# Performance work log

Hardware: AMD Instinct MI355X
Metric: run time of the kernel (lower is better)

The kernel has to match this reference:

```python
import jax, jax.numpy as jnp
import numpy as np

D_MODEL = 768
D_STATE = 128
EXPAND = 2
HEADDIM = 64
D_INNER = D_MODEL * EXPAND          # 1536
NHEADS = D_INNER // HEADDIM         # 24
CONV_K = 4
D_IN_PROJ = 2 * D_INNER + 2 * D_STATE + NHEADS  # z, xBC, dt
EPS = 1e-5


def setup_inputs() -> dict:
    key = jax.random.key(0)
    ks = jax.random.split(key, 12)
    B, L = 4, 4096
    conv_ch = D_INNER + 2 * D_STATE
    inp = {
        "x": jax.random.normal(ks[0], (B, L, D_MODEL), dtype=jnp.float32),
        "ln_w": jnp.ones((D_MODEL,), jnp.float32),
        "ln_b": jnp.zeros((D_MODEL,), jnp.float32),
        "W_in": jax.random.normal(ks[1], (D_MODEL, D_IN_PROJ), jnp.float32) * (D_MODEL ** -0.5),
        "conv_w": jax.random.normal(ks[2], (conv_ch, 1, CONV_K), jnp.float32) * (CONV_K ** -0.5),
        "conv_b": jnp.zeros((conv_ch,), jnp.float32),
        "A_log": jnp.log(jnp.arange(1, NHEADS + 1, dtype=jnp.float32)),
        "D": jnp.ones((NHEADS,), jnp.float32),
        "dt_bias": jnp.log(jnp.expm1(jax.random.uniform(ks[3], (NHEADS,), jnp.float32, 1e-3, 0.1))),
        "norm_w": jnp.ones((D_INNER,), jnp.float32),
        "W_out": jax.random.normal(ks[4], (D_INNER, D_MODEL), jnp.float32) * (D_INNER ** -0.5),
    }
    return inp


def _layernorm(x, w, b):
    mu = jnp.mean(x, -1, keepdims=True)
    var = jnp.mean(jnp.square(x - mu), -1, keepdims=True)
    return (x - mu) * jax.lax.rsqrt(var + EPS) * w + b


def _causal_dw_conv(x, w, b):
    # x: (B, L, C), w: (C, 1, K) depthwise causal conv
    xt = jnp.transpose(x, (0, 2, 1))                      # (B, C, L)
    xt = jnp.pad(xt, ((0, 0), (0, 0), (CONV_K - 1, 0)))
    y = jax.lax.conv_general_dilated(
        xt, w, window_strides=(1,), padding="VALID",
        dimension_numbers=("NCH", "OIH", "NCH"),
        feature_group_count=x.shape[-1])
    return jnp.transpose(y, (0, 2, 1)) + b                # (B, L, C)


def _mamba_core(u, W_in, conv_w, conv_b, A_log, D, dt_bias, norm_w, W_out):
    Bsz, L, _ = u.shape
    zxbcdt = u @ W_in                                      # (B, L, D_IN_PROJ)
    z = zxbcdt[..., :D_INNER]
    xBC = zxbcdt[..., D_INNER:D_INNER + D_INNER + 2 * D_STATE]
    dt = zxbcdt[..., -NHEADS:]                             # (B, L, H)

    xBC = jax.nn.silu(_causal_dw_conv(xBC, conv_w, conv_b))
    xs = xBC[..., :D_INNER].reshape(Bsz, L, NHEADS, HEADDIM)   # (B,L,H,P)
    Bmat = xBC[..., D_INNER:D_INNER + D_STATE]                 # (B,L,N)
    Cmat = xBC[..., D_INNER + D_STATE:]                        # (B,L,N)

    dt = jax.nn.softplus(dt + dt_bias)                     # (B,L,H)
    A = -jnp.exp(A_log)                                    # (H,)
    dA = jnp.exp(dt * A)                                   # (B,L,H)

    def step(h, inputs):
        dA_t, dt_t, B_t, C_t, x_t = inputs                 # (B,H),(B,H),(B,N),(B,N),(B,H,P)
        h = dA_t[:, :, None, None] * h + \
            (dt_t[:, :, None] * x_t)[..., None] * B_t[:, None, None, :]
        y = jnp.einsum("bhpn,bn->bhp", h, C_t)
        return h, y

    h0 = jnp.zeros((Bsz, NHEADS, HEADDIM, D_STATE), u.dtype)
    seq = (jnp.moveaxis(dA, 1, 0), jnp.moveaxis(dt, 1, 0),
           jnp.moveaxis(Bmat, 1, 0), jnp.moveaxis(Cmat, 1, 0),
           jnp.moveaxis(xs, 1, 0))
    _, ys = jax.lax.scan(step, h0, seq)                    # (L,B,H,P)
    y = jnp.moveaxis(ys, 0, 1) + D[None, None, :, None] * xs
    y = y.reshape(Bsz, L, D_INNER)

    # gated RMSNorm then out projection
    yg = y * jax.nn.silu(z)
    yn = yg * jax.lax.rsqrt(jnp.mean(jnp.square(yg), -1, keepdims=True) + EPS) * norm_w
    return yn @ W_out


def reference(x, ln_w, ln_b, W_in, conv_w, conv_b, A_log, D, dt_bias, norm_w, W_out):
    u = _layernorm(x, ln_w, ln_b)
    out = _mamba_core(u, W_in, conv_w, conv_b, A_log, D, dt_bias, norm_w, W_out)
    return out + x  # dropout p=0.0 is identity
```

## Files before the change

kernel.cpp:

```cpp
#include <hip/hip_runtime.h>
#include <stdint.h>

#define B_SZ 4
#define LSEQ 4096
#define DMODEL 768
#define DSTATE 128
#define HEADD 64
#define DINNER 1536
#define NH 24
#define NPROJ 3352
#define NPROJ_PAD 3456
#define NXBC 1920
#define ROWS (B_SZ*LSEQ)
#define QC 64
#define NGRP 8
#define GQ 8
#define GLEN (GQ*QC)

typedef __attribute__((ext_vector_type(8))) short short8;
typedef __attribute__((ext_vector_type(4))) float floatx4;

__device__ __forceinline__ unsigned short f2bf(float f){
  union { float f; unsigned u; } v; v.f = f;
  unsigned r = v.u + 0x7FFFu + ((v.u >> 16) & 1u);
  return (unsigned short)(r >> 16);
}
__device__ __forceinline__ float bf2f(unsigned short u){
  union { unsigned u; float f; } v; v.u = ((unsigned)u) << 16; return v.f;
}
__device__ __forceinline__ float silu(float v){ return v / (1.f + __expf(-v)); }

__global__ __launch_bounds__(256) void transpose_bf16(const float* __restrict__ src, int R, int C,
                                                      unsigned short* __restrict__ dst){
  __shared__ __align__(16) float tile[32][33];
  int tx = threadIdx.x & 31, ty = threadIdx.x >> 5;
  int n0 = blockIdx.x * 32, k0 = blockIdx.y * 32;
  #pragma unroll
  for (int i = 0; i < 4; i++){
    int k = k0 + ty + i*8, n = n0 + tx;
    tile[ty + i*8][tx] = (n < C) ? src[(size_t)k * C + n] : 0.f;
  }
  __syncthreads();
  #pragma unroll
  for (int i = 0; i < 4; i++){
    int n = n0 + ty + i*8, k = k0 + tx;
    dst[(size_t)n * R + k] = f2bf(tile[tx][ty + i*8]);
  }
}

__global__ __launch_bounds__(256) void ln_kernel(const float* __restrict__ x, const float* __restrict__ w,
                                                 const float* __restrict__ b, unsigned short* __restrict__ u){
  int row = blockIdx.x, t = threadIdx.x;
  const float* xr = x + (size_t)row * DMODEL;
  float v0 = xr[t], v1 = xr[t+256], v2 = xr[t+512];
  float s = v0+v1+v2, ss = v0*v0+v1*v1+v2*v2;
  __shared__ float sa[4], sb[4];
  #pragma unroll
  for (int o = 32; o > 0; o >>= 1){ s += __shfl_down(s,o,64); ss += __shfl_down(ss,o,64); }
  if ((t & 63) == 0){ sa[t>>6] = s; sb[t>>6] = ss; }
  __syncthreads();
  s = sa[0]+sa[1]+sa[2]+sa[3]; ss = sb[0]+sb[1]+sb[2]+sb[3];
  float mu = s * (1.f/DMODEL);
  float var = ss * (1.f/DMODEL) - mu*mu;
  float rs = rsqrtf(var + 1e-5f);
  unsigned short* ur = u + (size_t)row * DMODEL;
  ur[t]     = f2bf((v0-mu)*rs*w[t]     + b[t]);
  ur[t+256] = f2bf((v1-mu)*rs*w[t+256] + b[t+256]);
  ur[t+512] = f2bf((v2-mu)*rs*w[t+512] + b[t+512]);
}

#define SSTR 1040
#define GEMM_CORE(A_, Bt_, K_)                                                          \
  __shared__ __align__(16) short As[4*SSTR];                                            \
  __shared__ __align__(16) short Bs[4*SSTR];                                            \
  int t = threadIdx.x;                                                                  \
  int bm = blockIdx.y, bn = blockIdx.x;                                                 \
  int wave = t >> 6, lane = t & 63;                                                     \
  int wr = wave >> 1, wc = wave & 1;                                                    \
  int q = lane >> 4, m16 = lane & 15;                                                   \
  floatx4 acc[4][4];                                                                    \
  _Pragma("unroll") for (int i=0;i<4;i++)                                               \
    _Pragma("unroll") for (int j=0;j<4;j++) acc[i][j] = (floatx4){0.f,0.f,0.f,0.f};     \
  const int r0 = t >> 2, s0 = t & 3;                                                    \
  for (int kt = 0; kt < (K_); kt += 32){                                                \
    uint4 av0 = *(const uint4*)((A_)  + (size_t)(bm*128 + r0     )*(K_) + kt + s0*8);   \
    uint4 av1 = *(const uint4*)((A_)  + (size_t)(bm*128 + r0 + 64)*(K_) + kt + s0*8);   \
    uint4 bv0 = *(const uint4*)((Bt_) + (size_t)(bn*128 + r0     )*(K_) + kt + s0*8);   \
    uint4 bv1 = *(const uint4*)((Bt_) + (size_t)(bn*128 + r0 + 64)*(K_) + kt + s0*8);   \
    *(uint4*)(As + s0*SSTR + r0*8)      = av0;                                          \
    *(uint4*)(As + s0*SSTR + (r0+64)*8) = av1;                                          \
    *(uint4*)(Bs + s0*SSTR + r0*8)      = bv0;                                          \
    *(uint4*)(Bs + s0*SSTR + (r0+64)*8) = bv1;                                          \
    __syncthreads();                                                                    \
    short8 af[4], bf_[4];                                                               \
    _Pragma("unroll") for (int i=0;i<4;i++){                                            \
      af[i]  = *(const short8*)(As + q*SSTR + (wr*64 + i*16 + m16)*8);                  \
      bf_[i] = *(const short8*)(Bs + q*SSTR + (wc*64 + i*16 + m16)*8);                  \
    }                                                                                   \
    _Pragma("unroll") for (int i=0;i<4;i++)                                             \
      _Pragma("unroll") for (int j=0;j<4;j++)                                           \
        acc[i][j] = __builtin_amdgcn_mfma_f32_16x16x32_bf16(af[i], bf_[j], acc[i][j], 0, 0, 0); \
    __syncthreads();                                                                    \
  }

__global__ __launch_bounds__(256) void gemm_in(const short* __restrict__ A, const short* __restrict__ Bt,
                                               unsigned short* __restrict__ zb, unsigned short* __restrict__ xb,
                                               float* __restrict__ dtb, const float* __restrict__ dt_bias){
  GEMM_CORE(A, Bt, DMODEL)
  #pragma unroll
  for (int i=0;i<4;i++){
    int grow_base = bm*128 + wr*64 + i*16 + q*4;
    #pragma unroll
    for (int j=0;j<4;j++){
      int gcol = bn*128 + wc*64 + j*16 + m16;
      #pragma unroll
      for (int r=0;r<4;r++){
        int row = grow_base + r;
        float v = acc[i][j][r];
        if (gcol < DINNER){
          zb[(size_t)row*DINNER + gcol] = f2bf(v);
        } else {
          xb[(size_t)row*NXBC + (gcol - DINNER)] = f2bf(v);
          if (gcol >= (NPROJ-NH) && gcol < NPROJ){
            int hh = gcol - (NPROJ-NH);
            float xr = v + dt_bias[hh];
            dtb[(size_t)row*NH + hh] = (xr > 20.f) ? xr : log1pf(expf(xr));
          }
        }
      }
    }
  }
}

__global__ __launch_bounds__(256) void gemm_out(const short* __restrict__ A, const short* __restrict__ Bt,
                                                float* __restrict__ C, const float* __restrict__ resid){
  GEMM_CORE(A, Bt, DINNER)
  #pragma unroll
  for (int i=0;i<4;i++){
    int grow_base = bm*128 + wr*64 + i*16 + q*4;
    #pragma unroll
    for (int j=0;j<4;j++){
      int gcol = bn*128 + wc*64 + j*16 + m16;
      #pragma unroll
      for (int r=0;r<4;r++){
        size_t idx = (size_t)(grow_base + r) * DMODEL + gcol;
        C[idx] = acc[i][j][r] + resid[idx];
      }
    }
  }
}

__global__ __launch_bounds__(256) void conv_bc(const unsigned short* __restrict__ xbc,
                                               const float* __restrict__ cw, const float* __restrict__ cb,
                                               unsigned short* __restrict__ bcv){
  int row = blockIdx.x, c = threadIdx.x;
  int l = row & (LSEQ-1);
  int chg = DINNER + c;
  float acc = cb[chg];
  #pragma unroll
  for (int k = 0; k < 4; k++){
    int ls = l + k - 3;
    if (ls >= 0) acc = fmaf(cw[chg*4+k], bf2f(xbc[(size_t)(row + k - 3)*NXBC + 1536 + c]), acc);
  }
  bcv[(size_t)row*256 + c] = f2bf(silu(acc));
}

__global__ __launch_bounds__(256, 2) void ssd_partial(const unsigned short* __restrict__ xbc,
                                                      const unsigned short* __restrict__ bcv,
                                                      const float* __restrict__ dtb,
                                                      const float* __restrict__ cw, const float* __restrict__ cb,
                                                      const float* __restrict__ A_log, const float* __restrict__ Dp,
                                                      unsigned short* __restrict__ yb,
                                                      unsigned short* __restrict__ gstate,
                                                      float* __restrict__ gamma){
  __shared__ __align__(16) unsigned short sBl[QC][136];
  __shared__ __align__(16) unsigned short sCl[QC][136];
  __shared__ __align__(16) unsigned short sXT[HEADD][72];
  __shared__ __align__(16) unsigned short sMR[67*72];
  __shared__ __align__(16) unsigned short sH[HEADD][136];
  __shared__ float sSeg[QC], sDt[QC], sW[QC], sCum[QC];

  int bid = blockIdx.x;
  int g = bid % NGRP, bh = bid / NGRP;
  int h = bh % NH, b = bh / NH;
  int bseq = b * LSEQ;
  int tid = threadIdx.x;
  int wv = tid >> 6, ln = tid & 63, q = ln >> 4, l16 = ln & 15;
  float A_h = -__expf(A_log[h]);
  float Dh = Dp[h];

  float cwr[4][4], cbr[4];
  #pragma unroll
  for (int sl = 0; sl < 4; sl++){
    int chg = h*HEADD + (tid>>4) + 16*sl;
    #pragma unroll
    for (int k = 0; k < 4; k++) cwr[sl][k] = cw[chg*4+k];
    cbr[sl] = cb[chg];
  }

  for (int i = tid; i < HEADD*136/2; i += 256) ((unsigned*)sH)[i] = 0u;
  floatx4 hacc[8];
  #pragma unroll
  for (int i = 0; i < 8; i++) hacc[i] = (floatx4){0.f,0.f,0.f,0.f};
  float segRun = 0.f;

  for (int cc = 0; cc < GQ; cc++){
    int l0 = g*GLEN + cc*QC;
    {
      int r = tid >> 2, gb = tid & 3;
      const unsigned short* bcrow = bcv + (size_t)(bseq + l0 + r)*256;
      uint4 bcl[8];
      #pragma unroll
      for (int j = 0; j < 8; j++) bcl[j] = *(const uint4*)(bcrow + (gb + 4*j)*8);
      uint4 rxl[3]; int rrow[3], rg[3]; bool rv[3];
      #pragma unroll
      for (int j = 0; j < 3; j++){
        int idx = tid + 256*j;
        rv[j] = idx < 536;
        int rr = idx >> 3, gg = idx & 7;
        rrow[j] = rr; rg[j] = gg;
        rxl[j] = (uint4){0,0,0,0};
        if (rv[j]){
          int gl = l0 + rr - 3;
          if (gl >= 0) rxl[j] = *(const uint4*)(xbc + (size_t)(bseq + gl)*NXBC + h*HEADD + gg*8);
        }
      }
      if (wv == 0){
        float dtv = dtb[(size_t)(bseq + l0 + ln)*NH + h];
        float sg = dtv * A_h;
        #pragma unroll
        for (int off = 1; off < 64; off <<= 1){
          float o = __shfl_up(sg, off, 64);
          sg += (ln >= off) ? o : 0.f;
        }
        float segLast = __shfl(sg, 63, 64);
        sSeg[ln] = sg; sDt[ln] = dtv;
        sW[ln] = dtv * __expf(segLast - sg);
        sCum[ln] = __expf(sg);
        gamma[(size_t)bh*LSEQ + l0 + ln] = __expf(segRun + sg);
        segRun += segLast;
      }
      #pragma unroll
      for (int j = 0; j < 8; j++){
        int ch0 = (gb + 4*j) * 8;
        if (ch0 < 128) *(uint4*)&sBl[r][ch0] = bcl[j];
        else           *(uint4*)&sCl[r][ch0-128] = bcl[j];
      }
      #pragma unroll
      for (int j = 0; j < 3; j++)
        if (rv[j]) *(uint4*)&sMR[rrow[j]*72 + rg[j]*8] = rxl[j];
    }
    __syncthreads();
    short8 cf[4];
    #pragma unroll
    for (int kt = 0; kt < 4; kt++) cf[kt] = *(const short8*)&sCl[16*wv + l16][kt*32 + q*8];
    floatx4 gacc[4];
    #pragma unroll
    for (int st = 0; st < 4; st++) gacc[st] = (floatx4){0.f,0.f,0.f,0.f};
    #pragma unroll
    for (int kt = 0; kt < 4; kt++){
      #pragma unroll
      for (int st = 0; st < 4; st++){
        short8 bfr = *(const short8*)&sBl[16*st + l16][kt*32 + q*8];
        gacc[st] = __builtin_amdgcn_mfma_f32_16x16x32_bf16(cf[kt], bfr, gacc[st], 0, 0, 0);
      }
    }
    {
      int s4 = (tid & 15) * 4;
      #pragma unroll
      for (int sl = 0; sl < 4; sl++){
        int ch = (tid >> 4) + 16*sl;
        float rr[7];
        #pragma unroll
        for (int k = 0; k < 7; k++) rr[k] = bf2f(sMR[(s4 + k)*72 + ch]);
        #pragma unroll
        for (int i = 0; i < 4; i++){
          float v = cbr[sl] + cwr[sl][0]*rr[i] + cwr[sl][1]*rr[i+1] + cwr[sl][2]*rr[i+2] + cwr[sl][3]*rr[i+3];
          sXT[ch][s4+i] = f2bf(silu(v));
        }
      }
    }
    __syncthreads();
    #pragma unroll
    for (int st = 0; st < 4; st++){
      #pragma unroll
      for (int r = 0; r < 4; r++){
        int tt = 16*wv + q*4 + r;
        int ss = 16*st + l16;
        float mv = 0.f;
        if (ss <= tt) mv = __expf(sSeg[tt] - sSeg[ss]) * sDt[ss] * gacc[st][r];
        sMR[tt*72 + ss] = f2bf(mv);
      }
    }
    __syncthreads();
    short8 xf[2][4];
    #pragma unroll
    for (int kt = 0; kt < 2; kt++)
      #pragma unroll
      for (int pt = 0; pt < 4; pt++)
        xf[kt][pt] = *(const short8*)&sXT[16*pt + l16][kt*32 + q*8];
    floatx4 yac[4], y2[4];
    #pragma unroll
    for (int pt = 0; pt < 4; pt++){ yac[pt] = (floatx4){0,0,0,0}; y2[pt] = (floatx4){0,0,0,0}; }
    #pragma unroll
    for (int kt = 0; kt < 2; kt++){
      short8 mf = *(const short8*)&sMR[(16*wv + l16)*72 + kt*32 + q*8];
      #pragma unroll
      for (int pt = 0; pt < 4; pt++)
        yac[pt] = __builtin_amdgcn_mfma_f32_16x16x32_bf16(mf, xf[kt][pt], yac[pt], 0, 0, 0);
    }
    #pragma unroll
    for (int kt = 0; kt < 4; kt++){
      #pragma unroll
      for (int pt = 0; pt < 4; pt++){
        short8 hf = *(const short8*)&sH[16*pt + l16][kt*32 + q*8];
        y2[pt] = __builtin_amdgcn_mfma_f32_16x16x32_bf16(cf[kt], hf, y2[pt], 0, 0, 0);
      }
    }
    float P = sCum[QC-1];
    #pragma unroll
    for (int i = 0; i < 8; i++) hacc[i] *= P;
    #pragma unroll
    for (int kt = 0; kt < 2; kt++){
      float4 w0 = *(const float4*)&sW[kt*32 + q*8];
      float4 w1 = *(const float4*)&sW[kt*32 + q*8 + 4];
      float wsc[8] = { w0.x, w0.y, w0.z, w0.w, w1.x, w1.y, w1.z, w1.w };
      short8 bt0, bt1;
      #pragma unroll
      for (int jj = 0; jj < 8; jj++){
        int srow = kt*32 + q*8 + jj;
        bt0[jj] = (short)f2bf(bf2f(sBl[srow][32*wv + l16])      * wsc[jj]);
        bt1[jj] = (short)f2bf(bf2f(sBl[srow][32*wv + 16 + l16]) * wsc[jj]);
      }
      #pragma unroll
      for (int pt = 0; pt < 4; pt++){
        hacc[pt*2+0] = __builtin_amdgcn_mfma_f32_16x16x32_bf16(xf[kt][pt], bt0, hacc[pt*2+0], 0, 0, 0);
        hacc[pt*2+1] = __builtin_amdgcn_mfma_f32_16x16x32_bf16(xf[kt][pt], bt1, hacc[pt*2+1], 0, 0, 0);
      }
    }
    #pragma unroll
    for (int r = 0; r < 4; r++){
      int trow = 16*wv + q*4 + r;
      float cum_t = sCum[trow];
      size_t gbase = (size_t)(bseq + l0 + trow)*DINNER + h*HEADD;
      #pragma unroll
      for (int pt = 0; pt < 4; pt++){
        float xv = bf2f(sXT[16*pt + l16][trow]);
        yb[gbase + 16*pt + l16] = f2bf(yac[pt][r] + cum_t * y2[pt][r] + Dh * xv);
      }
    }
    __syncthreads();
    #pragma unroll
    for (int pt = 0; pt < 4; pt++)
      #pragma unroll
      for (int nt = 0; nt < 2; nt++)
        #pragma unroll
        for (int r = 0; r < 4; r++)
          sH[16*pt + q*4 + r][32*wv + 16*nt + l16] = f2bf(hacc[pt*2+nt][r]);
  }
  #pragma unroll
  for (int pt = 0; pt < 4; pt++)
    #pragma unroll
    for (int nt = 0; nt < 2; nt++)
      #pragma unroll
      for (int r = 0; r < 4; r++)
        gstate[(size_t)bid*8192 + (16*pt + q*4 + r)*128 + 32*wv + 16*nt + l16] = f2bf(hacc[pt*2+nt][r]);
}

__global__ __launch_bounds__(512) void combine_groups(unsigned short* __restrict__ gstate,
                                                      const float* __restrict__ gamma){
  int bh = blockIdx.x;
  int t = threadIdx.x;
  size_t off = (size_t)(t >> 3)*128 + (t & 7)*16;
  float hr[16];
  #pragma unroll
  for (int i = 0; i < 16; i++) hr[i] = 0.f;
  for (int g = 0; g < NGRP; g++){
    unsigned short* ptr = gstate + (size_t)(bh*NGRP + g)*8192 + off;
    union { uint4 v; unsigned short s[8]; } a0, a1, b0, b1;
    a0.v = *(const uint4*)ptr; a1.v = *(const uint4*)(ptr + 8);
    float P = gamma[(size_t)bh*LSEQ + g*GLEN + (GLEN-1)];
    #pragma unroll
    for (int i = 0; i < 8; i++){ b0.s[i] = f2bf(hr[i]); b1.s[i] = f2bf(hr[8+i]); }
    *(uint4*)ptr = b0.v; *(uint4*)(ptr + 8) = b1.v;
    #pragma unroll
    for (int i = 0; i < 8; i++){
      hr[i]   = fmaf(P, hr[i],   bf2f(a0.s[i]));
      hr[8+i] = fmaf(P, hr[8+i], bf2f(a1.s[i]));
    }
  }
}

__global__ __launch_bounds__(256) void ssd_fixup(const unsigned short* __restrict__ bcv,
                                                 const unsigned short* __restrict__ gstate,
                                                 const float* __restrict__ gamma,
                                                 unsigned short* __restrict__ yb){
  __shared__ __align__(16) unsigned short sHf[HEADD][136];
  int bid = blockIdx.x;
  int g = bid % NGRP, bh = bid / NGRP;
  int h = bh % NH, b = bh / NH;
  int bseq = b * LSEQ;
  int tid = threadIdx.x, wv = tid >> 6, ln = tid & 63, q = ln >> 4, l16 = ln & 15;
  {
    int p = tid >> 2, n0 = (tid & 3) * 32;
    const unsigned short* src = gstate + (size_t)bid*8192 + p*128 + n0;
    uint4 v0 = *(const uint4*)(src);     uint4 v1 = *(const uint4*)(src + 8);
    uint4 v2 = *(const uint4*)(src + 16); uint4 v3 = *(const uint4*)(src + 24);
    *(uint4*)&sHf[p][n0]      = v0; *(uint4*)&sHf[p][n0 + 8]  = v1;
    *(uint4*)&sHf[p][n0 + 16] = v2; *(uint4*)&sHf[p][n0 + 24] = v3;
  }
  __syncthreads();
  short8 hf[4][4];
  #pragma unroll
  for (int pt = 0; pt < 4; pt++)
    #pragma unroll
    for (int kt = 0; kt < 4; kt++)
      hf[pt][kt] = *(const short8*)&sHf[16*pt + l16][kt*32 + q*8];
  for (int it = 0; it < 8; it++){
    int lrow = g*GLEN + (it*4 + wv)*16;
    short8 cf2[4];
    #pragma unroll
    for (int kt = 0; kt < 4; kt++)
      cf2[kt] = *(const short8*)(bcv + (size_t)(bseq + lrow + l16)*256 + 128 + kt*32 + q*8);
    floatx4 y2[4];
    #pragma unroll
    for (int pt = 0; pt < 4; pt++) y2[pt] = (floatx4){0,0,0,0};
    #pragma unroll
    for (int kt = 0; kt < 4; kt++)
      #pragma unroll
      for (int pt = 0; pt < 4; pt++)
        y2[pt] = __builtin_amdgcn_mfma_f32_16x16x32_bf16(cf2[kt], hf[pt][kt], y2[pt], 0, 0, 0);
    #pragma unroll
    for (int r = 0; r < 4; r++){
      float gv = gamma[(size_t)bh*LSEQ + lrow + q*4 + r];
      size_t ybase = (size_t)(bseq + lrow + q*4 + r)*DINNER + h*HEADD;
      #pragma unroll
      for (int pt = 0; pt < 4; pt++){
        size_t ci = ybase + 16*pt + l16;
        yb[ci] = f2bf(bf2f(yb[ci]) + gv * y2[pt][r]);
      }
    }
  }
}

__global__ __launch_bounds__(256) void gate_rms(const unsigned short* __restrict__ y,
                                                const unsigned short* __restrict__ z,
                                                const float* __restrict__ nw, unsigned short* __restrict__ yn){
  int row = blockIdx.x, t = threadIdx.x;
  const unsigned short* yr = y + (size_t)row*DINNER;
  const unsigned short* zr = z + (size_t)row*DINNER;
  float g[6]; float ss = 0.f;
  #pragma unroll
  for (int i=0;i<6;i++){
    int c2 = t + i*256;
    float zv = bf2f(zr[c2]);
    float gv = bf2f(yr[c2]) * silu(zv);
    g[i] = gv; ss += gv*gv;
  }
  __shared__ float sb_[4];
  #pragma unroll
  for (int o = 32; o > 0; o >>= 1) ss += __shfl_down(ss,o,64);
  if ((t & 63) == 0) sb_[t>>6] = ss;
  __syncthreads();
  ss = sb_[0]+sb_[1]+sb_[2]+sb_[3];
  float scale = rsqrtf(ss*(1.f/DINNER) + 1e-5f);
  unsigned short* ynr = yn + (size_t)row*DINNER;
  #pragma unroll
  for (int i=0;i<6;i++){
    int c2 = t + i*256;
    ynr[c2] = f2bf(g[i]*scale*nw[c2]);
  }
}

extern "C" void kernel_launch(void* const* d_in, const int* in_sizes, int n_in,
                              void* d_out, int out_size, void* d_ws, size_t ws_size,
                              hipStream_t stream){
  const float* x      = (const float*)d_in[0];
  const float* ln_w   = (const float*)d_in[1];
  const float* ln_b   = (const float*)d_in[2];
  const float* W_in   = (const float*)d_in[3];
  const float* conv_w = (const float*)d_in[4];
  const float* conv_b = (const float*)d_in[5];
  const float* A_log  = (const float*)d_in[6];
  const float* Dp     = (const float*)d_in[7];
  const float* dt_b   = (const float*)d_in[8];
  const float* nw     = (const float*)d_in[9];
  const float* W_out  = (const float*)d_in[10];
  float* out = (float*)d_out;

  char* ws = (char*)d_ws;
  size_t off = 0;
  auto alloc = [&](size_t bytes)->char*{ char* pp = ws + off; off += (bytes + 255) & ~(size_t)255; return pp; };
  unsigned short* zbuf  = (unsigned short*)alloc((size_t)ROWS*DINNER*2);
  unsigned short* xbcdt = (unsigned short*)alloc((size_t)ROWS*NXBC*2);
  float* dtb   = (float*)alloc((size_t)ROWS*NH*4);
  float* gamma = (float*)alloc((size_t)B_SZ*NH*LSEQ*4);
  char* big0   = alloc((size_t)ROWS*DMODEL*2);
  char* big1   = alloc((size_t)B_SZ*NH*NGRP*HEADD*DSTATE*2);
  unsigned short* ybuf = (unsigned short*)alloc((size_t)ROWS*DINNER*2);
  unsigned short* woutT= (unsigned short*)alloc((size_t)DMODEL*DINNER*2);
  unsigned short* u_bf   = (unsigned short*)big0;
  unsigned short* bcconv = (unsigned short*)big0;
  unsigned short* winT   = (unsigned short*)big1;
  unsigned short* gstate = (unsigned short*)big1;
  unsigned short* ynb    = xbcdt;
  (void)ws_size; (void)in_sizes; (void)n_in; (void)out_size;

  transpose_bf16<<<dim3(NPROJ_PAD/32, DMODEL/32), 256, 0, stream>>>(W_in, DMODEL, NPROJ, winT);
  transpose_bf16<<<dim3(DMODEL/32, DINNER/32), 256, 0, stream>>>(W_out, DINNER, DMODEL, woutT);
  ln_kernel<<<ROWS, 256, 0, stream>>>(x, ln_w, ln_b, u_bf);
  gemm_in<<<dim3(NPROJ_PAD/128, ROWS/128), 256, 0, stream>>>((const short*)u_bf, (const short*)winT,
                                                             zbuf, xbcdt, dtb, dt_b);
  conv_bc<<<ROWS, 256, 0, stream>>>(xbcdt, conv_w, conv_b, bcconv);
  ssd_partial<<<B_SZ*NH*NGRP, 256, 0, stream>>>(xbcdt, bcconv, dtb, conv_w, conv_b,
                                                A_log, Dp, ybuf, gstate, gamma);
  combine_groups<<<B_SZ*NH, 512, 0, stream>>>(gstate, gamma);
  ssd_fixup<<<B_SZ*NH*NGRP, 256, 0, stream>>>(bcconv, gstate, gamma, ybuf);
  gate_rms<<<ROWS, 256, 0, stream>>>(ybuf, zbuf, nw, ynb);
  gemm_out<<<dim3(DMODEL/128, ROWS/128), 256, 0, stream>>>((const short*)ynb, (const short*)woutT,
                                                           out, x);
}
```

Baseline: 582.8 us.

## Load GEMM tiles directly into LDS and remap blocks for L2 locality

The GEMM core now uses global_load_lds (direct global-to-LDS 16-byte loads) instead of staging tiles through registers, which removes the VGPR round trip and LDS store instructions. Each wave loads one k-slice column of 64 rows into the strided LDS layout. Both GEMMs also switch to a 1D grid with a swizzled block mapping: gemm_in walks panels of 9 N-tiles across all M-tiles, and gemm_out uses row-major tile order, to improve L2 reuse of the weight and activation tiles. Direct-to-LDS loads on gfx950 need the wave-uniform LDS base and lane-contiguous layout to match; here a lane-by-16-byte layout is assumed.

New measurement: 654.4 us. 1.12x slower.

```diff
diff --git a/kernel.cpp b/kernel.cpp
--- a/kernel.cpp
+++ b/kernel.cpp
@@ -30,6 +30,11 @@
 }
 __device__ __forceinline__ float silu(float v){ return v / (1.f + __expf(-v)); }
 
+__device__ __forceinline__ void gld16(const void* g, void* l){
+  __builtin_amdgcn_global_load_lds((const __attribute__((address_space(1))) void*)g,
+                                   (__attribute__((address_space(3))) void*)l, 16, 0, 0);
+}
+
 __global__ __launch_bounds__(256) void transpose_bf16(const float* __restrict__ src, int R, int C,
                                                       unsigned short* __restrict__ dst){
   __shared__ __align__(16) float tile[32][33];
@@ -71,26 +76,28 @@
 
 #define SSTR 1040
 #define GEMM_CORE(A_, Bt_, K_)                                                          \
-  __shared__ __align__(16) short As[4*SSTR];                                            \
-  __shared__ __align__(16) short Bs[4*SSTR];                                            \
+  __shared__ __align__(16) unsigned short As[4*SSTR];                                   \
+  __shared__ __align__(16) unsigned short Bs[4*SSTR];                                   \
   int t = threadIdx.x;                                                                  \
-  int bm = blockIdx.y, bn = blockIdx.x;                                                 \
   int wave = t >> 6, lane = t & 63;                                                     \
   int wr = wave >> 1, wc = wave & 1;                                                    \
   int q = lane >> 4, m16 = lane & 15;                                                   \
   floatx4 acc[4][4];                                                                    \
   _Pragma("unroll") for (int i=0;i<4;i++)                                               \
     _Pragma("unroll") for (int j=0;j<4;j++) acc[i][j] = (floatx4){0.f,0.f,0.f,0.f};     \
-  const int r0 = t >> 2, s0 = t & 3;                                                    \
+  const unsigned short* ga0 = (const unsigned short*)(A_)  + (size_t)(bm*128 + lane)*(K_) + wave*8; \
+  const unsigned short* ga1 = ga0 + (size_t)64*(K_);                                    \
+  const unsigned short* gb0 = (const unsigned short*)(Bt_) + (size_t)(bn*128 + lane)*(K_) + wave*8; \
+  const unsigned short* gb1 = gb0 + (size_t)64*(K_);                                    \
+  unsigned short* la0 = As + wave*SSTR;                                                 \
+  unsigned short* la1 = As + wave*SSTR + 512;                                           \
+  unsigned short* lb0 = Bs + wave*SSTR;                                                 \
+  unsigned short* lb1 = Bs + wave*SSTR + 512;                                           \
   for (int kt = 0; kt < (K_); kt += 32){                                                \
-    uint4 av0 = *(const uint4*)((A_)  + (size_t)(bm*128 + r0     )*(K_) + kt + s0*8);   \
-    uint4 av1 = *(const uint4*)((A_)  + (size_t)(bm*128 + r0 + 64)*(K_) + kt + s0*8);   \
-    uint4 bv0 = *(const uint4*)((Bt_) + (size_t)(bn*128 + r0     )*(K_) + kt + s0*8);   \
-    uint4 bv1 = *(const uint4*)((Bt_) + (size_t)(bn*128 + r0 + 64)*(K_) + kt + s0*8);   \
-    *(uint4*)(As + s0*SSTR + r0*8)      = av0;                                          \
-    *(uint4*)(As + s0*SSTR + (r0+64)*8) = av1;                                          \
-    *(uint4*)(Bs + s0*SSTR + r0*8)      = bv0;                                          \
-    *(uint4*)(Bs + s0*SSTR + (r0+64)*8) = bv1;                                          \
+    gld16(ga0 + kt, la0);                                                               \
+    gld16(ga1 + kt, la1);                                                               \
+    gld16(gb0 + kt, lb0);                                                               \
+    gld16(gb1 + kt, lb1);                                                               \
     __syncthreads();                                                                    \
     short8 af[4], bf_[4];                                                               \
     _Pragma("unroll") for (int i=0;i<4;i++){                                            \
@@ -106,6 +113,11 @@
 __global__ __launch_bounds__(256) void gemm_in(const short* __restrict__ A, const short* __restrict__ Bt,
                                                unsigned short* __restrict__ zb, unsigned short* __restrict__ xb,
                                                float* __restrict__ dtb, const float* __restrict__ dt_bias){
+  int id = blockIdx.x;
+  int panel = id / (128*9);
+  int within = id - panel*(128*9);
+  int bm = within / 9;
+  int bn = panel*9 + (within - bm*9);
   GEMM_CORE(A, Bt, DMODEL)
   #pragma unroll
   for (int i=0;i<4;i++){
@@ -134,6 +146,9 @@
 
 __global__ __launch_bounds__(256) void gemm_out(const short* __restrict__ A, const short* __restrict__ Bt,
                                                 float* __restrict__ C, const float* __restrict__ resid){
+  int id = blockIdx.x;
+  int bm = id / 6;
+  int bn = id - bm*6;
   GEMM_CORE(A, Bt, DINNER)
   #pragma unroll
   for (int i=0;i<4;i++){
@@ -509,14 +524,14 @@
   transpose_bf16<<<dim3(NPROJ_PAD/32, DMODEL/32), 256, 0, stream>>>(W_in, DMODEL, NPROJ, winT);
   transpose_bf16<<<dim3(DMODEL/32, DINNER/32), 256, 0, stream>>>(W_out, DINNER, DMODEL, woutT);
   ln_kernel<<<ROWS, 256, 0, stream>>>(x, ln_w, ln_b, u_bf);
-  gemm_in<<<dim3(NPROJ_PAD/128, ROWS/128), 256, 0, stream>>>((const short*)u_bf, (const short*)winT,
-                                                             zbuf, xbcdt, dtb, dt_b);
+  gemm_in<<<3456, 256, 0, stream>>>((const short*)u_bf, (const short*)winT,
+                                    zbuf, xbcdt, dtb, dt_b);
   conv_bc<<<ROWS, 256, 0, stream>>>(xbcdt, conv_w, conv_b, bcconv);
   ssd_partial<<<B_SZ*NH*NGRP, 256, 0, stream>>>(xbcdt, bcconv, dtb, conv_w, conv_b,
                                                 A_log, Dp, ybuf, gstate, gamma);
   combine_groups<<<B_SZ*NH, 512, 0, stream>>>(gstate, gamma);
   ssd_fixup<<<B_SZ*NH*NGRP, 256, 0, stream>>>(bcconv, gstate, gamma, ybuf);
   gate_rms<<<ROWS, 256, 0, stream>>>(ybuf, zbuf, nw, ynb);
-  gemm_out<<<dim3(DMODEL/128, ROWS/128), 256, 0, stream>>>((const short*)ynb, (const short*)woutT,
-                                                           out, x);
-}
+  gemm_out<<<768, 256, 0, stream>>>((const short*)ynb, (const short*)woutT,
+                                    out, x);
+}
```
